# Kernel tuning notes

Measured on AMD Instinct MI355X. Metric: run time of the kernel, lower is better.

## Reference

```python
import jax, jax.numpy as jnp
import numpy as np

B, S, E, H = 32, 2048, 256, 256

def setup_inputs() -> dict:
    key = jax.random.key(0)
    ks = jax.random.split(key, 8)
    scale = 1.0 / np.sqrt(H)  # kaiming-uniform-ish magnitude
    return {
        "x": jax.random.normal(ks[0], (B, S, E), dtype=jnp.float32),
        "h0": jax.random.normal(ks[1], (B, H), dtype=jnp.float32),
        "Wz": jax.random.normal(ks[2], (E, H), dtype=jnp.float32) * scale,
        "Uz": jax.random.normal(ks[3], (H, H), dtype=jnp.float32) * scale,
        "Wr": jax.random.normal(ks[4], (E, H), dtype=jnp.float32) * scale,
        "Ur": jax.random.normal(ks[5], (H, H), dtype=jnp.float32) * scale,
        "Wh": jax.random.normal(ks[6], (E, H), dtype=jnp.float32) * scale,
        "Uh": jax.random.normal(ks[7], (H, H), dtype=jnp.float32) * scale,
    }

def reference(x, h0, Wz, Uz, Wr, Ur, Wh, Uh):
    # Precompute input-side projections for all timesteps in three big GEMMs,
    # then scan the recurrence over time. Math identical to the per-step loop.
    xz = jnp.einsum('bse,eh->sbh', x, Wz)  # [S,B,H]
    xr = jnp.einsum('bse,eh->sbh', x, Wr)
    xh = jnp.einsum('bse,eh->sbh', x, Wh)

    def step(h, inp):
        xz_t, xr_t, xh_t = inp
        z = jax.nn.sigmoid(xz_t + h @ Uz)
        r = jax.nn.sigmoid(xr_t + h @ Ur)
        h_wave = jnp.tanh(xh_t + (r * h) @ Uh)
        h_new = (1.0 - z) * h + z * h_wave
        return h_new, h_new

    _, Ht = jax.lax.scan(step, h0, (xz, xr, xh))  # Ht: [S,B,H]
    return jnp.transpose(Ht, (1, 0, 2))  # [B,S,H]
```

## Files before the change

### kernel.cpp

```cpp
#include <hip/hip_runtime.h>

typedef _Float16 f16;
typedef _Float16 f16x2 __attribute__((ext_vector_type(2)));
typedef _Float16 f16x8 __attribute__((ext_vector_type(8)));
typedef __fp16   h16x2 __attribute__((ext_vector_type(2)));
typedef float    f32x4 __attribute__((ext_vector_type(4)));

#define B_ 32
#define S_ 2048
#define E_ 256
#define H_ 256
#define M_ (B_ * S_)

union U32F2 { unsigned int u; f16x2 h; h16x2 g; };

__device__ __forceinline__ float fdot2f(f16x2 a, f16x2 b, float c) {
#if __has_builtin(__builtin_amdgcn_fdot2)
  return __builtin_amdgcn_fdot2(a, b, c, false);
#else
  return c + (float)a.x * (float)b.x + (float)a.y * (float)b.y;
#endif
}
__device__ __forceinline__ float fdot2u(unsigned int w, unsigned int v, float c) {
  U32F2 a, b; a.u = w; b.u = v;
  return fdot2f(a.h, b.h, c);
}

__device__ __forceinline__ float fast_exp2(float x) {
#if __has_builtin(__builtin_amdgcn_exp2f)
  return __builtin_amdgcn_exp2f(x);
#else
  return exp2f(x);
#endif
}
__device__ __forceinline__ float fast_rcp(float x) {
#if __has_builtin(__builtin_amdgcn_rcpf)
  return __builtin_amdgcn_rcpf(x);
#else
  return 1.0f / x;
#endif
}
__device__ __forceinline__ float sigm(float x) {
  float e = fast_exp2(-1.4426950408889634f * x);
  return fast_rcp(1.0f + e);
}
__device__ __forceinline__ float tanh_fast(float x) {
  x = fminf(15.0f, fmaxf(-15.0f, x));
  float e = fast_exp2(2.8853900817779268f * x);
  return (e - 1.0f) * fast_rcp(e + 1.0f);
}

__global__ __launch_bounds__(256, 4) void proj_gemm(
    const float* __restrict__ x, const float* __restrict__ Wz,
    const float* __restrict__ Wr, const float* __restrict__ Wh,
    f16* __restrict__ Xg) {
  __shared__ __align__(16) f16 Wl[64][264];
  const int tid = threadIdx.x;
  const int wv = tid >> 6;
  const int ln = tid & 63;
  const int M0 = blockIdx.x * 64;
  const int nb = blockIdx.y;
  const int gate = nb >> 2;
  const int c0 = (nb & 3) * 64;
  const float* W = (gate == 0) ? Wz : (gate == 1 ? Wr : Wh);

#pragma unroll
  for (int i = 0; i < 64; ++i) {
    int e = i * 256 + tid;
    int cl = e & 63;
    int k = e >> 6;
    Wl[cl][k] = (f16)W[(size_t)k * H_ + c0 + cl];
  }
  __syncthreads();

  const int row = M0 + wv * 16 + (ln & 15);
  const int kg = (ln >> 4) * 8;
  f32x4 acc0 = {0.f, 0.f, 0.f, 0.f};
  f32x4 acc1 = {0.f, 0.f, 0.f, 0.f};
  f32x4 acc2 = {0.f, 0.f, 0.f, 0.f};
  f32x4 acc3 = {0.f, 0.f, 0.f, 0.f};

#pragma unroll
  for (int kk = 0; kk < 8; ++kk) {
    const int k0 = kk * 32;
    const float* ap = x + (size_t)row * E_ + k0 + kg;
    float4 a0 = *(const float4*)ap;
    float4 a1 = *(const float4*)(ap + 4);
    f16x8 af = {(f16)a0.x, (f16)a0.y, (f16)a0.z, (f16)a0.w,
                (f16)a1.x, (f16)a1.y, (f16)a1.z, (f16)a1.w};
    f16x8 b0 = *(const f16x8*)&Wl[0 * 16 + (ln & 15)][k0 + kg];
    f16x8 b1 = *(const f16x8*)&Wl[1 * 16 + (ln & 15)][k0 + kg];
    f16x8 b2 = *(const f16x8*)&Wl[2 * 16 + (ln & 15)][k0 + kg];
    f16x8 b3 = *(const f16x8*)&Wl[3 * 16 + (ln & 15)][k0 + kg];
    acc0 = __builtin_amdgcn_mfma_f32_16x16x32_f16(af, b0, acc0, 0, 0, 0);
    acc1 = __builtin_amdgcn_mfma_f32_16x16x32_f16(af, b1, acc1, 0, 0, 0);
    acc2 = __builtin_amdgcn_mfma_f32_16x16x32_f16(af, b2, acc2, 0, 0, 0);
    acc3 = __builtin_amdgcn_mfma_f32_16x16x32_f16(af, b3, acc3, 0, 0, 0);
  }

  f16* outg = Xg + (size_t)gate * ((size_t)M_ * H_);
  const int rbase = M0 + wv * 16 + (ln >> 4) * 4;
#define EPI(NT, ACC)                                                       \
  {                                                                        \
    const int cc = c0 + NT * 16 + (ln & 15);                               \
    outg[(size_t)(rbase + 0) * H_ + cc] = (f16)ACC[0];                     \
    outg[(size_t)(rbase + 1) * H_ + cc] = (f16)ACC[1];                     \
    outg[(size_t)(rbase + 2) * H_ + cc] = (f16)ACC[2];                     \
    outg[(size_t)(rbase + 3) * H_ + cc] = (f16)ACC[3];                     \
  }
  EPI(0, acc0) EPI(1, acc1) EPI(2, acc2) EPI(3, acc3)
#undef EPI
}

__global__ __launch_bounds__(1024) void gru_rec(
    const f16* __restrict__ Xg, const float* __restrict__ h0,
    const float* __restrict__ Uz, const float* __restrict__ Ur,
    const float* __restrict__ Uh, float* __restrict__ out) {
  __shared__ __align__(16) unsigned int h2v[4 * 36];
  __shared__ __align__(16) unsigned int rh2v[4 * 36];
  const int b = blockIdx.x;
  const int tid = threadIdx.x;
  const int wv = tid >> 6;
  const int ln = tid & 63;
  const int c = wv * 16 + (ln & 15);
  const int kq = ln >> 4;
  const bool owner = (kq == 0);

  unsigned int wzU[32], wrU[32], whU[32];
  {
    const int rb = kq * 64;
#pragma unroll
    for (int j = 0; j < 32; ++j) {
      const size_t o0 = (size_t)(rb + 2 * j) * H_ + c;
      U32F2 pz, pr, ph;
      pz.h = f16x2{(f16)Uz[o0], (f16)Uz[o0 + H_]};
      pr.h = f16x2{(f16)Ur[o0], (f16)Ur[o0 + H_]};
      ph.h = f16x2{(f16)Uh[o0], (f16)Uh[o0 + H_]};
      wzU[j] = pz.u; wrU[j] = pr.u; whU[j] = ph.u;
    }
  }
#pragma unroll
  for (int j = 0; j < 32; ++j) {
    asm("" : "+v"(wzU[j]));
    asm("" : "+v"(wrU[j]));
    asm("" : "+v"(whU[j]));
  }

  float h_reg = 0.f;
  if (owner) h_reg = h0[b * H_ + c];
  {
    float hn = __shfl_xor(h_reg, 1);
    if (owner && !(ln & 1)) {
      U32F2 p; p.g = __builtin_amdgcn_cvt_pkrtz(h_reg, hn);
      const int pi = c >> 1;
      h2v[(pi >> 5) * 36 + (pi & 31)] = p.u;
    }
  }
  __syncthreads();

  const f16* xz = Xg + (size_t)b * ((size_t)S_ * H_) + c;
  const f16* xr = xz + (size_t)M_ * H_;
  const f16* xh = xr + (size_t)M_ * H_;
  float* outp = out + (size_t)b * ((size_t)S_ * H_) + c;

  f16 pz = xz[0], pr = xr[0], ph = xh[0];

  const uint4* hq = (const uint4*)(h2v + kq * 36);
  const uint4* rq = (const uint4*)(rh2v + kq * 36);

  for (int t = 0; t < S_; ++t) {
    const float xzc = (float)pz, xrc = (float)pr, xhc = (float)ph;
    {
      const int t2 = (t + 1 < S_) ? (t + 1) : t;
      const size_t off = (size_t)t2 * H_;
      pz = xz[off]; pr = xr[off]; ph = xh[off];
    }

    float az = 0.f, ar = 0.f;
#pragma unroll
    for (int i = 0; i < 8; ++i) {
      uint4 hv = hq[i];
      az = fdot2u(wzU[4 * i + 0], hv.x, az);
      az = fdot2u(wzU[4 * i + 1], hv.y, az);
      az = fdot2u(wzU[4 * i + 2], hv.z, az);
      az = fdot2u(wzU[4 * i + 3], hv.w, az);
      ar = fdot2u(wrU[4 * i + 0], hv.x, ar);
      ar = fdot2u(wrU[4 * i + 1], hv.y, ar);
      ar = fdot2u(wrU[4 * i + 2], hv.z, ar);
      ar = fdot2u(wrU[4 * i + 3], hv.w, ar);
    }
    az += __shfl_xor(az, 16); az += __shfl_xor(az, 32);
    ar += __shfl_xor(ar, 16); ar += __shfl_xor(ar, 32);

    float z_s = 0.f, rh = 0.f;
    if (owner) {
      z_s = sigm(az + xzc);
      float rr = sigm(ar + xrc);
      rh = rr * h_reg;
    }
    {
      float rhn = __shfl_xor(rh, 1);
      if (owner && !(ln & 1)) {
        U32F2 p; p.g = __builtin_amdgcn_cvt_pkrtz(rh, rhn);
        const int pi = c >> 1;
        rh2v[(pi >> 5) * 36 + (pi & 31)] = p.u;
      }
    }
    __syncthreads();

    float ah0 = 0.f, ah1 = 0.f;
#pragma unroll
    for (int i = 0; i < 8; ++i) {
      uint4 rv = rq[i];
      ah0 = fdot2u(whU[4 * i + 0], rv.x, ah0);
      ah1 = fdot2u(whU[4 * i + 1], rv.y, ah1);
      ah0 = fdot2u(whU[4 * i + 2], rv.z, ah0);
      ah1 = fdot2u(whU[4 * i + 3], rv.w, ah1);
    }
    float ah = ah0 + ah1;
    ah += __shfl_xor(ah, 16); ah += __shfl_xor(ah, 32);

    if (owner) {
      float ht = tanh_fast(ah + xhc);
      h_reg = h_reg + z_s * (ht - h_reg);
      outp[(size_t)t * H_] = h_reg;
    }
    {
      float hn = __shfl_xor(h_reg, 1);
      if (owner && !(ln & 1)) {
        U32F2 p; p.g = __builtin_amdgcn_cvt_pkrtz(h_reg, hn);
        const int pi = c >> 1;
        h2v[(pi >> 5) * 36 + (pi & 31)] = p.u;
      }
    }
    __syncthreads();
  }
}

extern "C" void kernel_launch(void* const* d_in, const int* in_sizes, int n_in,
                              void* d_out, int out_size, void* d_ws,
                              size_t ws_size, hipStream_t stream) {
  const float* x  = (const float*)d_in[0];
  const float* h0 = (const float*)d_in[1];
  const float* Wz = (const float*)d_in[2];
  const float* Uz = (const float*)d_in[3];
  const float* Wr = (const float*)d_in[4];
  const float* Ur = (const float*)d_in[5];
  const float* Wh = (const float*)d_in[6];
  const float* Uh = (const float*)d_in[7];
  float* out = (float*)d_out;

  const size_t need = (size_t)3 * M_ * H_ * sizeof(f16);
  if (ws_size < need) return;
  f16* Xg = (f16*)d_ws;

  proj_gemm<<<dim3(M_ / 64, 12), 256, 0, stream>>>(x, Wz, Wr, Wh, Xg);
  gru_rec<<<dim3(B_), 1024, 0, stream>>>(Xg, h0, Uz, Ur, Uh, out);
}
```

Baseline: 3.633 ms.

## Halve recurrence block size by computing two hidden columns per thread

The GRU recurrence kernel now runs with 512 threads per block. Each thread owns two hidden columns (c and c+128) and keeps twice as many packed f16 recurrent weights in registers. This is meant to reduce per-step barrier and wave-synchronisation cost and expose more independent dot-product chains. A large shared array is allocated, apparently to force one block per compute unit. Register pressure per thread roughly doubles, which risks spills or lower scheduling flexibility.

```diff
diff --git a/kernel.cpp b/kernel.cpp
--- a/kernel.cpp
+++ b/kernel.cpp
@@ -112,12 +112,14 @@
 #undef EPI
 }
 
-__global__ __launch_bounds__(1024) void gru_rec(
+__global__ __launch_bounds__(512) void gru_rec(
     const f16* __restrict__ Xg, const float* __restrict__ h0,
     const float* __restrict__ Uz, const float* __restrict__ Ur,
     const float* __restrict__ Uh, float* __restrict__ out) {
-  __shared__ __align__(16) unsigned int h2v[4 * 36];
-  __shared__ __align__(16) unsigned int rh2v[4 * 36];
+  __shared__ __align__(16) unsigned int lds[24576];
+  unsigned int* h2v = lds;
+  unsigned int* rh2v = lds + 160;
+
   const int b = blockIdx.x;
   const int tid = threadIdx.x;
   const int wv = tid >> 6;
@@ -126,34 +128,43 @@
   const int kq = ln >> 4;
   const bool owner = (kq == 0);
 
-  unsigned int wzU[32], wrU[32], whU[32];
+  unsigned int wz0[32], wz1[32], wr0[32], wr1[32], wh0[32], wh1[32];
   {
     const int rb = kq * 64;
 #pragma unroll
     for (int j = 0; j < 32; ++j) {
-      const size_t o0 = (size_t)(rb + 2 * j) * H_ + c;
-      U32F2 pz, pr, ph;
-      pz.h = f16x2{(f16)Uz[o0], (f16)Uz[o0 + H_]};
-      pr.h = f16x2{(f16)Ur[o0], (f16)Ur[o0 + H_]};
-      ph.h = f16x2{(f16)Uh[o0], (f16)Uh[o0 + H_]};
-      wzU[j] = pz.u; wrU[j] = pr.u; whU[j] = ph.u;
+      const size_t o = (size_t)(rb + 2 * j) * H_ + c;
+      U32F2 t;
+      t.h = f16x2{(f16)Uz[o], (f16)Uz[o + H_]};             wz0[j] = t.u;
+      t.h = f16x2{(f16)Uz[o + 128], (f16)Uz[o + H_ + 128]}; wz1[j] = t.u;
+      t.h = f16x2{(f16)Ur[o], (f16)Ur[o + H_]};             wr0[j] = t.u;
+      t.h = f16x2{(f16)Ur[o + 128], (f16)Ur[o + H_ + 128]}; wr1[j] = t.u;
+      t.h = f16x2{(f16)Uh[o], (f16)Uh[o + H_]};             wh0[j] = t.u;
+      t.h = f16x2{(f16)Uh[o + 128], (f16)Uh[o + H_ + 128]}; wh1[j] = t.u;
     }
   }
 #pragma unroll
   for (int j = 0; j < 32; ++j) {
-    asm("" : "+v"(wzU[j]));
-    asm("" : "+v"(wrU[j]));
-    asm("" : "+v"(whU[j]));
-  }
-
-  float h_reg = 0.f;
-  if (owner) h_reg = h0[b * H_ + c];
+    asm("" : "+v"(wz0[j])); asm("" : "+v"(wz1[j]));
+    asm("" : "+v"(wr0[j])); asm("" : "+v"(wr1[j]));
+    asm("" : "+v"(wh0[j])); asm("" : "+v"(wh1[j]));
+  }
+
+  float h_reg0 = 0.f, h_reg1 = 0.f;
+  if (owner) {
+    h_reg0 = h0[b * H_ + c];
+    h_reg1 = h0[b * H_ + c + 128];
+  }
   {
-    float hn = __shfl_xor(h_reg, 1);
+    float hn0 = __shfl_xor(h_reg0, 1);
+    float hn1 = __shfl_xor(h_reg1, 1);
     if (owner && !(ln & 1)) {
-      U32F2 p; p.g = __builtin_amdgcn_cvt_pkrtz(h_reg, hn);
-      const int pi = c >> 1;
-      h2v[(pi >> 5) * 36 + (pi & 31)] = p.u;
+      U32F2 p0, p1;
+      p0.g = __builtin_amdgcn_cvt_pkrtz(h_reg0, hn0);
+      p1.g = __builtin_amdgcn_cvt_pkrtz(h_reg1, hn1);
+      const int pi0 = c >> 1, pi1 = (c >> 1) + 64;
+      h2v[(pi0 >> 5) * 36 + (pi0 & 31)] = p0.u;
+      h2v[(pi1 >> 5) * 36 + (pi1 & 31)] = p1.u;
     }
   }
   __syncthreads();
@@ -163,74 +174,107 @@
   const f16* xh = xr + (size_t)M_ * H_;
   float* outp = out + (size_t)b * ((size_t)S_ * H_) + c;
 
-  f16 pz = xz[0], pr = xr[0], ph = xh[0];
+  f16 pz0 = 0, pr0 = 0, ph0 = 0, pz1 = 0, pr1 = 0, ph1 = 0;
+  if (owner) {
+    pz0 = xz[0]; pr0 = xr[0]; ph0 = xh[0];
+    pz1 = xz[128]; pr1 = xr[128]; ph1 = xh[128];
+  }
 
   const uint4* hq = (const uint4*)(h2v + kq * 36);
   const uint4* rq = (const uint4*)(rh2v + kq * 36);
 
   for (int t = 0; t < S_; ++t) {
-    const float xzc = (float)pz, xrc = (float)pr, xhc = (float)ph;
-    {
+    const float xz0c = (float)pz0, xr0c = (float)pr0, xh0c = (float)ph0;
+    const float xz1c = (float)pz1, xr1c = (float)pr1, xh1c = (float)ph1;
+    if (owner) {
       const int t2 = (t + 1 < S_) ? (t + 1) : t;
       const size_t off = (size_t)t2 * H_;
-      pz = xz[off]; pr = xr[off]; ph = xh[off];
-    }
-
-    float az = 0.f, ar = 0.f;
+      pz0 = xz[off]; pr0 = xr[off]; ph0 = xh[off];
+      pz1 = xz[off + 128]; pr1 = xr[off + 128]; ph1 = xh[off + 128];
+    }
+
+    float az0 = 0.f, az1 = 0.f, ar0 = 0.f, ar1 = 0.f;
 #pragma unroll
     for (int i = 0; i < 8; ++i) {
       uint4 hv = hq[i];
-      az = fdot2u(wzU[4 * i + 0], hv.x, az);
-      az = fdot2u(wzU[4 * i + 1], hv.y, az);
-      az = fdot2u(wzU[4 * i + 2], hv.z, az);
-      az = fdot2u(wzU[4 * i + 3], hv.w, az);
-      ar = fdot2u(wrU[4 * i + 0], hv.x, ar);
-      ar = fdot2u(wrU[4 * i + 1], hv.y, ar);
-      ar = fdot2u(wrU[4 * i + 2], hv.z, ar);
-      ar = fdot2u(wrU[4 * i + 3], hv.w, ar);
-    }
-    az += __shfl_xor(az, 16); az += __shfl_xor(az, 32);
-    ar += __shfl_xor(ar, 16); ar += __shfl_xor(ar, 32);
-
-    float z_s = 0.f, rh = 0.f;
+      az0 = fdot2u(wz0[4 * i + 0], hv.x, az0);
+      az0 = fdot2u(wz0[4 * i + 1], hv.y, az0);
+      az0 = fdot2u(wz0[4 * i + 2], hv.z, az0);
+      az0 = fdot2u(wz0[4 * i + 3], hv.w, az0);
+      az1 = fdot2u(wz1[4 * i + 0], hv.x, az1);
+      az1 = fdot2u(wz1[4 * i + 1], hv.y, az1);
+      az1 = fdot2u(wz1[4 * i + 2], hv.z, az1);
+      az1 = fdot2u(wz1[4 * i + 3], hv.w, az1);
+      ar0 = fdot2u(wr0[4 * i + 0], hv.x, ar0);
+      ar0 = fdot2u(wr0[4 * i + 1], hv.y, ar0);
+      ar0 = fdot2u(wr0[4 * i + 2], hv.z, ar0);
+      ar0 = fdot2u(wr0[4 * i + 3], hv.w, ar0);
+      ar1 = fdot2u(wr1[4 * i + 0], hv.x, ar1);
+      ar1 = fdot2u(wr1[4 * i + 1], hv.y, ar1);
+      ar1 = fdot2u(wr1[4 * i + 2], hv.z, ar1);
+      ar1 = fdot2u(wr1[4 * i + 3], hv.w, ar1);
+    }
+    az0 += __shfl_xor(az0, 16); az0 += __shfl_xor(az0, 32);
+    az1 += __shfl_xor(az1, 16); az1 += __shfl_xor(az1, 32);
+    ar0 += __shfl_xor(ar0, 16); ar0 += __shfl_xor(ar0, 32);
+    ar1 += __shfl_xor(ar1, 16); ar1 += __shfl_xor(ar1, 32);
+
+    float z0 = 0.f, z1 = 0.f, rh0 = 0.f, rh1 = 0.f;
     if (owner) {
-      z_s = sigm(az + xzc);
-      float rr = sigm(ar + xrc);
-      rh = rr * h_reg;
+      z0 = sigm(az0 + xz0c);
+      z1 = sigm(az1 + xz1c);
+      rh0 = sigm(ar0 + xr0c) * h_reg0;
+      rh1 = sigm(ar1 + xr1c) * h_reg1;
     }
     {
-      float rhn = __shfl_xor(rh, 1);
+      float rn0 = __shfl_xor(rh0, 1);
+      float rn1 = __shfl_xor(rh1, 1);
       if (owner && !(ln & 1)) {
-        U32F2 p; p.g = __builtin_amdgcn_cvt_pkrtz(rh, rhn);
-        const int pi = c >> 1;
-        rh2v[(pi >> 5) * 36 + (pi & 31)] = p.u;
+        U32F2 p0, p1;
+        p0.g = __builtin_amdgcn_cvt_pkrtz(rh0, rn0);
+        p1.g = __builtin_amdgcn_cvt_pkrtz(rh1, rn1);
+        const int pi0 = c >> 1, pi1 = (c >> 1) + 64;
+        rh2v[(pi0 >> 5) * 36 + (pi0 & 31)] = p0.u;
+        rh2v[(pi1 >> 5) * 36 + (pi1 & 31)] = p1.u;
       }
     }
     __syncthreads();
 
-    float ah0 = 0.f, ah1 = 0.f;
+    float a0a = 0.f, a0b = 0.f, a1a = 0.f, a1b = 0.f;
 #pragma unroll
     for (int i = 0; i < 8; ++i) {
       uint4 rv = rq[i];
-      ah0 = fdot2u(whU[4 * i + 0], rv.x, ah0);
-      ah1 = fdot2u(whU[4 * i + 1], rv.y, ah1);
-      ah0 = fdot2u(whU[4 * i + 2], rv.z, ah0);
-      ah1 = fdot2u(whU[4 * i + 3], rv.w, ah1);
-    }
-    float ah = ah0 + ah1;
-    ah += __shfl_xor(ah, 16); ah += __shfl_xor(ah, 32);
+      a0a = fdot2u(wh0[4 * i + 0], rv.x, a0a);
+      a0b = fdot2u(wh0[4 * i + 1], rv.y, a0b);
+      a0a = fdot2u(wh0[4 * i + 2], rv.z, a0a);
+      a0b = fdot2u(wh0[4 * i + 3], rv.w, a0b);
+      a1a = fdot2u(wh1[4 * i + 0], rv.x, a1a);
+      a1b = fdot2u(wh1[4 * i + 1], rv.y, a1b);
+      a1a = fdot2u(wh1[4 * i + 2], rv.z, a1a);
+      a1b = fdot2u(wh1[4 * i + 3], rv.w, a1b);
+    }
+    float ah0 = a0a + a0b, ah1 = a1a + a1b;
+    ah0 += __shfl_xor(ah0, 16); ah0 += __shfl_xor(ah0, 32);
+    ah1 += __shfl_xor(ah1, 16); ah1 += __shfl_xor(ah1, 32);
 
     if (owner) {
-      float ht = tanh_fast(ah + xhc);
-      h_reg = h_reg + z_s * (ht - h_reg);
-      outp[(size_t)t * H_] = h_reg;
+      float ht0 = tanh_fast(ah0 + xh0c);
+      float ht1 = tanh_fast(ah1 + xh1c);
+      h_reg0 = h_reg0 + z0 * (ht0 - h_reg0);
+      h_reg1 = h_reg1 + z1 * (ht1 - h_reg1);
+      outp[(size_t)t * H_] = h_reg0;
+      outp[(size_t)t * H_ + 128] = h_reg1;
     }
     {
-      float hn = __shfl_xor(h_reg, 1);
+      float hn0 = __shfl_xor(h_reg0, 1);
+      float hn1 = __shfl_xor(h_reg1, 1);
       if (owner && !(ln & 1)) {
-        U32F2 p; p.g = __builtin_amdgcn_cvt_pkrtz(h_reg, hn);
-        const int pi = c >> 1;
-        h2v[(pi >> 5) * 36 + (pi & 31)] = p.u;
+        U32F2 p0, p1;
+        p0.g = __builtin_amdgcn_cvt_pkrtz(h_reg0, hn0);
+        p1.g = __builtin_amdgcn_cvt_pkrtz(h_reg1, hn1);
+        const int pi0 = c >> 1, pi1 = (c >> 1) + 64;
+        h2v[(pi0 >> 5) * 36 + (pi0 & 31)] = p0.u;
+        h2v[(pi1 >> 5) * 36 + (pi1 & 31)] = p1.u;
       }
     }
     __syncthreads();
@@ -255,5 +299,5 @@
   f16* Xg = (f16*)d_ws;
 
   proj_gemm<<<dim3(M_ / 64, 12), 256, 0, stream>>>(x, Wz, Wr, Wh, Xg);
-  gru_rec<<<dim3(B_), 1024, 0, stream>>>(Xg, h0, Uz, Ur, Uh, out);
-}
+  gru_rec<<<dim3(B_), 512, 0, stream>>>(Xg, h0, Uz, Ur, Uh, out);
+}
```

After: 3.382 ms. -6.9%, faster.
